# Kernel tuning notes

Measured on AMD Instinct MI355X. Metric: run time of the kernel, lower is better.

## Reference

```python
import jax, jax.numpy as jnp
import numpy as np

IMG = 800.0
STRIDES = (4, 8, 16, 32)
SIZES = (32.0, 64.0, 128.0, 256.0)
RATIOS = (0.5, 1.0, 2.0)
A = 3
PRE_NMS_K = 1000
POST_NMS = 512
NMS_TH = 0.7
POOL = 7
_MEAN = np.array([0.485, 0.456, 0.406], np.float32).reshape(3, 1, 1)
_STD = np.array([0.229, 0.224, 0.225], np.float32).reshape(3, 1, 1)


def _conv(x, w, stride=1):
    # x: [C,H,W], w: [O,I,kh,kw]
    return jax.lax.conv_general_dilated(x[None], w, (stride, stride), 'SAME',
                                        dimension_numbers=('NCHW', 'OIHW', 'NCHW'))[0]


def _make_anchors(fh, fw, stride, size):
    cy = (np.arange(fh, dtype=np.float32) + 0.5) * stride
    cx = (np.arange(fw, dtype=np.float32) + 0.5) * stride
    ws = np.array([size / np.sqrt(r) for r in RATIOS], np.float32)
    hs = np.array([size * np.sqrt(r) for r in RATIOS], np.float32)
    gy, gx = np.meshgrid(cy, cx, indexing='ij')
    x1 = gx[..., None] - ws / 2; y1 = gy[..., None] - hs / 2
    x2 = gx[..., None] + ws / 2; y2 = gy[..., None] + hs / 2
    return jnp.asarray(np.stack([x1, y1, x2, y2], -1).reshape(-1, 4))  # [fh*fw*A,4]


def _decode(anchors, deltas):
    aw = anchors[:, 2] - anchors[:, 0]; ah = anchors[:, 3] - anchors[:, 1]
    acx = anchors[:, 0] + aw * 0.5; acy = anchors[:, 1] + ah * 0.5
    dw = jnp.clip(deltas[:, 2], -4.0, 4.0); dh = jnp.clip(deltas[:, 3], -4.0, 4.0)
    cx = acx + deltas[:, 0] * aw; cy = acy + deltas[:, 1] * ah
    w = aw * jnp.exp(dw); h = ah * jnp.exp(dh)
    boxes = jnp.stack([cx - w * 0.5, cy - h * 0.5, cx + w * 0.5, cy + h * 0.5], -1)
    return jnp.clip(boxes, 0.0, IMG)


def _nms(boxes, scores, iou_th, max_out):
    # Greedy NMS with fixed output size (jit-compatible).
    x1, y1, x2, y2 = boxes[:, 0], boxes[:, 1], boxes[:, 2], boxes[:, 3]
    areas = (x2 - x1) * (y2 - y1)

    def body(i, state):
        s, keep = state
        idx = jnp.argmax(s)
        keep = keep.at[i].set(idx)
        ix1 = jnp.maximum(x1, x1[idx]); iy1 = jnp.maximum(y1, y1[idx])
        ix2 = jnp.minimum(x2, x2[idx]); iy2 = jnp.minimum(y2, y2[idx])
        inter = jnp.maximum(ix2 - ix1, 0.0) * jnp.maximum(iy2 - iy1, 0.0)
        iou = inter / (areas + areas[idx] - inter + 1e-6)
        return jnp.where(iou > iou_th, -jnp.inf, s), keep

    _, keep = jax.lax.fori_loop(0, max_out, body, (scores, jnp.zeros(max_out, jnp.int32)))
    return keep


def _roi_align(feat, rois, scale):
    # feat: [C,H,W]; rois: [N,4] in image coords; bilinear, 1 sample per bin.
    C, H, W = feat.shape
    n = rois.shape[0]
    x1 = rois[:, 0] * scale; y1 = rois[:, 1] * scale
    bw = (rois[:, 2] - rois[:, 0]) * scale / POOL
    bh = (rois[:, 3] - rois[:, 1]) * scale / POOL
    j = jnp.arange(POOL, dtype=feat.dtype) + 0.5
    gx = jnp.broadcast_to((x1[:, None] + j * bw[:, None] - 0.5)[:, None, :], (n, POOL, POOL))
    gy = jnp.broadcast_to((y1[:, None] + j * bh[:, None] - 0.5)[:, :, None], (n, POOL, POOL))
    fx = jnp.clip(jnp.floor(gx), 0.0, W - 1); fy = jnp.clip(jnp.floor(gy), 0.0, H - 1)
    x0 = fx.astype(jnp.int32); y0 = fy.astype(jnp.int32)
    x1i = jnp.minimum(x0 + 1, W - 1); y1i = jnp.minimum(y0 + 1, H - 1)
    wx = jnp.clip(gx - fx, 0.0, 1.0); wy = jnp.clip(gy - fy, 0.0, 1.0)
    v = (feat[:, y0, x0] * (1 - wy) * (1 - wx) + feat[:, y0, x1i] * (1 - wy) * wx
         + feat[:, y1i, x0] * wy * (1 - wx) + feat[:, y1i, x1i] * wy * wx)  # [C,N,P,P]
    return jnp.transpose(v, (1, 0, 2, 3))  # [N,C,P,P]


def _forward(x, stem_w, c2_w, c3_w, c4_w, c5_w, fpn2_w, fpn3_w, fpn4_w, fpn5_w,
             rpn_w, rpn_cls_w, rpn_box_w, fc1_w, fc1_b, fc2_w, fc2_b,
             cls_w, cls_b, breg_w, breg_b):
    x = (x - _MEAN) / _STD  # ImageNet normalize
    h = jax.nn.relu(_conv(x, stem_w, 2))      # [64,400,400]
    c2 = jax.nn.relu(_conv(h, c2_w, 2))       # [256,200,200] stride 4
    c3 = jax.nn.relu(_conv(c2, c3_w, 2))      # stride 8
    c4 = jax.nn.relu(_conv(c3, c4_w, 2))      # stride 16
    c5 = jax.nn.relu(_conv(c4, c5_w, 2))      # stride 32
    feats = [_conv(c2, fpn2_w), _conv(c3, fpn3_w), _conv(c4, fpn4_w), _conv(c5, fpn5_w)]

    boxes_l, scores_l = [], []
    for lvl, f in enumerate(feats):
        t = jax.nn.relu(_conv(f, rpn_w))
        fh, fw = f.shape[1], f.shape[2]
        logits = jnp.transpose(_conv(t, rpn_cls_w), (1, 2, 0)).reshape(-1)  # [fh*fw*A]
        deltas = jnp.transpose(_conv(t, rpn_box_w).reshape(A, 4, fh, fw), (2, 3, 0, 1)).reshape(-1, 4)
        anchors = _make_anchors(fh, fw, STRIDES[lvl], SIZES[lvl])
        dec = _decode(anchors, deltas)
        k = min(PRE_NMS_K, logits.shape[0])
        sc, idx = jax.lax.top_k(logits, k)
        boxes_l.append(dec[idx]); scores_l.append(sc)

    boxes = jnp.concatenate(boxes_l, 0)
    scores = jnp.concatenate(scores_l, 0)
    keep = _nms(boxes, scores, NMS_TH, POST_NMS)
    props = boxes[keep]  # [POST_NMS,4]

    pooled = _roi_align(feats[0], props, 1.0 / STRIDES[0])  # [N,256,7,7]
    v = pooled.reshape(POST_NMS, -1)
    v = jax.nn.relu(v @ fc1_w + fc1_b)
    v = jax.nn.relu(v @ fc2_w + fc2_b)
    return v @ cls_w + cls_b, v @ breg_w + breg_b, props, scores[keep]


def setup_inputs() -> dict:
    key = jax.random.key(0)
    ks = jax.random.split(key, 18)

    def he(k, shape):
        fan_in = int(np.prod(shape[1:])) if len(shape) == 4 else shape[0]
        return jax.random.normal(k, shape, jnp.float32) * float(np.sqrt(2.0 / fan_in))

    inp = {'x': jax.random.uniform(ks[0], (3, 800, 800), jnp.float32)}
    inp['stem_w'] = he(ks[1], (64, 3, 7, 7))
    inp['c2_w'] = he(ks[2], (256, 64, 3, 3))
    for i, name in enumerate(['c3_w', 'c4_w', 'c5_w', 'fpn2_w', 'fpn3_w', 'fpn4_w', 'fpn5_w', 'rpn_w']):
        inp[name] = he(ks[3 + i], (256, 256, 3, 3))
    inp['rpn_cls_w'] = he(ks[11], (3, 256, 1, 1))
    inp['rpn_box_w'] = he(ks[12], (12, 256, 1, 1))
    inp['fc1_w'] = he(ks[13], (12544, 1024)); inp['fc1_b'] = jnp.zeros((1024,), jnp.float32)
    inp['fc2_w'] = he(ks[14], (1024, 1024)); inp['fc2_b'] = jnp.zeros((1024,), jnp.float32)
    inp['cls_w'] = he(ks[15], (1024, 2)); inp['cls_b'] = jnp.zeros((2,), jnp.float32)
    inp['breg_w'] = he(ks[16], (1024, 8)); inp['breg_b'] = jnp.zeros((8,), jnp.float32)
    return inp


def reference(x, stem_w, c2_w, c3_w, c4_w, c5_w, fpn2_w, fpn3_w, fpn4_w, fpn5_w,
              rpn_w, rpn_cls_w, rpn_box_w, fc1_w, fc1_b, fc2_w, fc2_b,
              cls_w, cls_b, breg_w, breg_b):
    return _forward(x, stem_w, c2_w, c3_w, c4_w, c5_w, fpn2_w, fpn3_w, fpn4_w, fpn5_w,
                    rpn_w, rpn_cls_w, rpn_box_w, fc1_w, fc1_b, fc2_w, fc2_b,
                    cls_w, cls_b, breg_w, breg_b)
```

## Files before the change

### kernel.cpp

```cpp
#include <hip/hip_runtime.h>
#include <math.h>


#define DI __device__ __forceinline__

typedef short short8 __attribute__((ext_vector_type(8)));
typedef float float16v __attribute__((ext_vector_type(16)));

DI unsigned fkey(float f) {
  unsigned u = __float_as_uint(f);
  return (u & 0x80000000u) ? ~u : (u | 0x80000000u);
}

DI unsigned short f2bf(float f) {
  unsigned u = __float_as_uint(f);
  unsigned r = (u + 0x7FFFu + ((u >> 16) & 1u)) >> 16;
  return (unsigned short)r;
}

__global__ __launch_bounds__(256) void stem_conv(const float* __restrict__ x,
                                                 const float* __restrict__ w,
                                                 float* __restrict__ out) {
  __shared__ float tin[3 * 37 * 37];
  __shared__ float tw[4 * 147];
  const int x0 = blockIdx.x * 16, y0 = blockIdx.y * 16, co0 = blockIdx.z * 4;
  const int tid = threadIdx.x;
  for (int i = tid; i < 4 * 147; i += 256) tw[i] = w[co0 * 147 + i];
  const int ix0 = x0 * 2 - 2, iy0 = y0 * 2 - 2;
  const float mean[3] = {0.485f, 0.456f, 0.406f};
  const float stdv[3] = {0.229f, 0.224f, 0.225f};
  for (int i = tid; i < 3 * 37 * 37; i += 256) {
    int c = i / 1369, r = i % 1369, yy = r / 37, xx = r % 37;
    int gy = iy0 + yy, gx = ix0 + xx;
    float v = 0.f;
    if ((unsigned)gy < 800u && (unsigned)gx < 800u)
      v = __fdiv_rn(__fsub_rn(x[c * 640000 + gy * 800 + gx], mean[c]), stdv[c]);
    tin[i] = v;
  }
  __syncthreads();
  const int tx = tid & 15, ty = tid >> 4;
  float acc[4] = {0.f, 0.f, 0.f, 0.f};
  for (int c = 0; c < 3; ++c)
    for (int ky = 0; ky < 7; ++ky)
#pragma unroll
      for (int kx = 0; kx < 7; ++kx) {
        float v = tin[c * 1369 + (ty * 2 + ky) * 37 + (tx * 2 + kx)];
#pragma unroll
        for (int co = 0; co < 4; ++co)
          acc[co] = fmaf(v, tw[co * 147 + c * 49 + ky * 7 + kx], acc[co]);
      }
  int ox = x0 + tx, oy = y0 + ty;
#pragma unroll
  for (int co = 0; co < 4; ++co)
    out[(size_t)(co0 + co) * 160000 + oy * 400 + ox] = fmaxf(acc[co], 0.f);
}

__global__ void repack_w32(const float* __restrict__ w,
                           float* __restrict__ wpk, int Cin) {
  int i = blockIdx.x * 256 + threadIdx.x;
  int total = 16 * Cin * 9 * 16;
  if (i >= total) return;
  int co = i & 15;
  int r = i >> 4;
  int kk = r % 9;
  int r2 = r / 9;
  int ci = r2 % Cin;
  int z = r2 / Cin;
  wpk[i] = w[((size_t)(z * 16 + co) * Cin + ci) * 9 + kk];
}

template <int CHUNK, bool RELU>
__global__ __launch_bounds__(256) void conv32_db(
    const float* __restrict__ in, const float* __restrict__ wpk,
    float* __restrict__ out, int Cin, int Hin, int Win, int Hout, int Wout) {
  constexpr int TILE = CHUNK * 612;
  constexpr int NS = (TILE + 255) / 256;
  constexpr int PADT = NS * 256;
  __shared__ __align__(16) float tin2[2][PADT];
  const int tid = threadIdx.x;
  const int tx = tid & 15, ty = tid >> 4;
  const int x0 = blockIdx.x * 32, y0 = blockIdx.y * 16;
  const int ix0 = x0 - 1, iy0 = y0 - 1;
  const size_t HWin = (size_t)Hin * Win;

  int goff[NS];
#pragma unroll
  for (int j = 0; j < NS; ++j) {
    int e = j * 256 + tid;
    int c = e / 612, r = e % 612;
    int yy = r / 34, xx = r % 34;
    int gy = iy0 + yy, gx = ix0 + xx;
    bool ok = (e < TILE) && ((unsigned)gy < (unsigned)Hin) &&
              ((unsigned)gx < (unsigned)Win);
    goff[j] = ok ? (int)((size_t)c * HWin + (size_t)gy * Win + gx) : -1;
  }

  float acc0[16], acc1[16];
#pragma unroll
  for (int co = 0; co < 16; ++co) { acc0[co] = 0.f; acc1[co] = 0.f; }

  float stg[NS];
#pragma unroll
  for (int j = 0; j < NS; ++j)
    stg[j] = (goff[j] >= 0) ? in[goff[j]] : 0.f;
#pragma unroll
  for (int j = 0; j < NS; ++j) tin2[0][j * 256 + tid] = stg[j];
  __syncthreads();

  int buf = 0;
  for (int cb = 0; cb < Cin; cb += CHUNK) {
    const bool more = (cb + CHUNK) < Cin;
    if (more) {
      const float* gsrc = in + (size_t)(cb + CHUNK) * HWin;
#pragma unroll
      for (int j = 0; j < NS; ++j)
        stg[j] = (goff[j] >= 0) ? gsrc[goff[j]] : 0.f;
    }
    for (int ci = 0; ci < CHUNK; ++ci) {
      const float4* wq = (const float4*)(wpk +
          ((size_t)blockIdx.z * Cin + (size_t)(cb + ci)) * 144);
#pragma unroll
      for (int ky = 0; ky < 3; ++ky) {
        const float* tb = &tin2[buf][ci * 612 + (ty + ky) * 34 + 2 * tx];
        float2 d0 = *(const float2*)tb;
        float2 d1 = *(const float2*)(tb + 2);
#pragma unroll
        for (int kx = 0; kx < 3; ++kx) {
          float v0 = (kx == 0) ? d0.x : (kx == 1) ? d0.y : d1.x;
          float v1 = (kx == 0) ? d0.y : (kx == 1) ? d1.x : d1.y;
          const int kk = ky * 3 + kx;
          float4 w0 = wq[kk * 4 + 0];
          float4 w1 = wq[kk * 4 + 1];
          float4 w2 = wq[kk * 4 + 2];
          float4 w3 = wq[kk * 4 + 3];
          acc0[0]  = fmaf(v0, w0.x, acc0[0]);
          acc0[1]  = fmaf(v0, w0.y, acc0[1]);
          acc0[2]  = fmaf(v0, w0.z, acc0[2]);
          acc0[3]  = fmaf(v0, w0.w, acc0[3]);
          acc1[0]  = fmaf(v1, w0.x, acc1[0]);
          acc1[1]  = fmaf(v1, w0.y, acc1[1]);
          acc1[2]  = fmaf(v1, w0.z, acc1[2]);
          acc1[3]  = fmaf(v1, w0.w, acc1[3]);
          acc0[4]  = fmaf(v0, w1.x, acc0[4]);
          acc0[5]  = fmaf(v0, w1.y, acc0[5]);
          acc0[6]  = fmaf(v0, w1.z, acc0[6]);
          acc0[7]  = fmaf(v0, w1.w, acc0[7]);
          acc1[4]  = fmaf(v1, w1.x, acc1[4]);
          acc1[5]  = fmaf(v1, w1.y, acc1[5]);
          acc1[6]  = fmaf(v1, w1.z, acc1[6]);
          acc1[7]  = fmaf(v1, w1.w, acc1[7]);
          acc0[8]  = fmaf(v0, w2.x, acc0[8]);
          acc0[9]  = fmaf(v0, w2.y, acc0[9]);
          acc0[10] = fmaf(v0, w2.z, acc0[10]);
          acc0[11] = fmaf(v0, w2.w, acc0[11]);
          acc1[8]  = fmaf(v1, w2.x, acc1[8]);
          acc1[9]  = fmaf(v1, w2.y, acc1[9]);
          acc1[10] = fmaf(v1, w2.z, acc1[10]);
          acc1[11] = fmaf(v1, w2.w, acc1[11]);
          acc0[12] = fmaf(v0, w3.x, acc0[12]);
          acc0[13] = fmaf(v0, w3.y, acc0[13]);
          acc0[14] = fmaf(v0, w3.z, acc0[14]);
          acc0[15] = fmaf(v0, w3.w, acc0[15]);
          acc1[12] = fmaf(v1, w3.x, acc1[12]);
          acc1[13] = fmaf(v1, w3.y, acc1[13]);
          acc1[14] = fmaf(v1, w3.z, acc1[14]);
          acc1[15] = fmaf(v1, w3.w, acc1[15]);
        }
      }
    }
    if (more) {
#pragma unroll
      for (int j = 0; j < NS; ++j) tin2[buf ^ 1][j * 256 + tid] = stg[j];
    }
    __syncthreads();
    buf ^= 1;
  }

  const int co0 = blockIdx.z * 16;
  int oy = y0 + ty;
  if (oy < Hout) {
    int ox = x0 + 2 * tx;
    if (ox + 1 < Wout) {
#pragma unroll
      for (int co = 0; co < 16; ++co) {
        float a = acc0[co], b = acc1[co];
        if (RELU) { a = fmaxf(a, 0.f); b = fmaxf(b, 0.f); }
        float2 st; st.x = a; st.y = b;
        *(float2*)&out[(size_t)(co0 + co) * Hout * Wout +
                       (size_t)oy * Wout + ox] = st;
      }
    } else if (ox < Wout) {
#pragma unroll
      for (int co = 0; co < 16; ++co) {
        float a = acc0[co];
        if (RELU) a = fmaxf(a, 0.f);
        out[(size_t)(co0 + co) * Hout * Wout + (size_t)oy * Wout + ox] = a;
      }
    }
  }
}

template <int CHUNK, bool RELU>
__global__ __launch_bounds__(256) void conv16_s1(const float* __restrict__ in,
                                                 const float* __restrict__ wpk,
                                                 float* __restrict__ out,
                                                 int Cin, int Hin, int Win,
                                                 int Hout, int Wout) {
  constexpr int P = 24;
  constexpr int TOT = CHUNK * 18 * 18;
  constexpr int NS = (TOT + 255) / 256;
  __shared__ __align__(16) float tin[CHUNK * 18 * P];
  const int tid = threadIdx.x;
  const int tx = tid & 15, ty = tid >> 4;
  const int x0 = blockIdx.x * 16, y0 = blockIdx.y * 16;
  const int ix0 = x0 - 1, iy0 = y0 - 1;
  const size_t HWin = (size_t)Hin * Win;

  int goff[NS], loff[NS];
#pragma unroll
  for (int j = 0; j < NS; ++j) {
    int i = tid + j * 256;
    int c = i / 324, r = i % 324;
    int yy = r / 18, xx = r % 18;
    int gy = iy0 + yy, gx = ix0 + xx;
    bool ok = (i < TOT) && ((unsigned)gy < (unsigned)Hin) &&
              ((unsigned)gx < (unsigned)Win);
    goff[j] = ok ? (int)(c * HWin + (size_t)gy * Win + gx) : -1;
    loff[j] = c * 18 * P + yy * P + xx;
  }

  float acc[16];
#pragma unroll
  for (int co = 0; co < 16; ++co) acc[co] = 0.f;

  for (int cb = 0; cb < Cin; cb += CHUNK) {
    const size_t gbase = (size_t)cb * HWin;
#pragma unroll
    for (int j = 0; j < NS; ++j) {
      int i = tid + j * 256;
      if (i < TOT) {
        float v = 0.f;
        if (goff[j] >= 0) v = in[gbase + goff[j]];
        tin[loff[j]] = v;
      }
    }
    __syncthreads();
    for (int ci = 0; ci < CHUNK; ++ci) {
      const float4* wq = (const float4*)(wpk +
          ((size_t)blockIdx.z * Cin + (size_t)(cb + ci)) * 144);
#pragma unroll
      for (int ky = 0; ky < 3; ++ky) {
#pragma unroll
        for (int kx = 0; kx < 3; ++kx) {
          const int kk = ky * 3 + kx;
          float v = tin[ci * 18 * P + (ty + ky) * P + tx + kx];
          float4 w0 = wq[kk * 4 + 0];
          float4 w1 = wq[kk * 4 + 1];
          float4 w2 = wq[kk * 4 + 2];
          float4 w3 = wq[kk * 4 + 3];
          acc[0]  = fmaf(v, w0.x, acc[0]);
          acc[1]  = fmaf(v, w0.y, acc[1]);
          acc[2]  = fmaf(v, w0.z, acc[2]);
          acc[3]  = fmaf(v, w0.w, acc[3]);
          acc[4]  = fmaf(v, w1.x, acc[4]);
          acc[5]  = fmaf(v, w1.y, acc[5]);
          acc[6]  = fmaf(v, w1.z, acc[6]);
          acc[7]  = fmaf(v, w1.w, acc[7]);
          acc[8]  = fmaf(v, w2.x, acc[8]);
          acc[9]  = fmaf(v, w2.y, acc[9]);
          acc[10] = fmaf(v, w2.z, acc[10]);
          acc[11] = fmaf(v, w2.w, acc[11]);
          acc[12] = fmaf(v, w3.x, acc[12]);
          acc[13] = fmaf(v, w3.y, acc[13]);
          acc[14] = fmaf(v, w3.z, acc[14]);
          acc[15] = fmaf(v, w3.w, acc[15]);
        }
      }
    }
    __syncthreads();
  }
  const int co0 = blockIdx.z * 16;
  int oy = y0 + ty, ox = x0 + tx;
  if (oy < Hout && ox < Wout) {
#pragma unroll
    for (int co = 0; co < 16; ++co) {
      float v = acc[co];
      if (RELU) v = fmaxf(v, 0.f);
      out[(size_t)(co0 + co) * Hout * Wout + (size_t)oy * Wout + ox] = v;
    }
  }
}

template <int CHUNK, bool RELU>
__global__ __launch_bounds__(256) void conv16_s2(const float* __restrict__ in,
                                                 const float* __restrict__ wpk,
                                                 float* __restrict__ out,
                                                 int Cin, int Hin, int Win,
                                                 int Hout, int Wout) {
  constexpr int P = 20;
  constexpr int HALF = CHUNK * 33 * P;
  constexpr int TOT = CHUNK * 33 * 33;
  constexpr int NS = (TOT + 255) / 256;
  __shared__ __align__(16) float tin2[2 * HALF];
  const int tid = threadIdx.x;
  const int tx = tid & 15, ty = tid >> 4;
  const int x0 = blockIdx.x * 16, y0 = blockIdx.y * 16;
  const int ix0 = x0 * 2, iy0 = y0 * 2;
  const size_t HWin = (size_t)Hin * Win;

  int goff[NS], loff[NS];
#pragma unroll
  for (int j = 0; j < NS; ++j) {
    int i = tid + j * 256;
    int c = i / 1089, r = i % 1089;
    int yy = r / 33, xx = r % 33;
    int gy = iy0 + yy, gx = ix0 + xx;
    bool ok = (i < TOT) && ((unsigned)gy < (unsigned)Hin) &&
              ((unsigned)gx < (unsigned)Win);
    goff[j] = ok ? (int)(c * HWin + (size_t)gy * Win + gx) : -1;
    loff[j] = c * 33 * P + yy * P + (xx >> 1) + ((xx & 1) ? HALF : 0);
  }

  float acc[16];
#pragma unroll
  for (int co = 0; co < 16; ++co) acc[co] = 0.f;

  for (int cb = 0; cb < Cin; cb += CHUNK) {
    const size_t gbase = (size_t)cb * HWin;
#pragma unroll
    for (int j = 0; j < NS; ++j) {
      int i = tid + j * 256;
      if (i < TOT) {
        float v = 0.f;
        if (goff[j] >= 0) v = in[gbase + goff[j]];
        tin2[loff[j]] = v;
      }
    }
    __syncthreads();
    for (int ci = 0; ci < CHUNK; ++ci) {
      const float4* wq = (const float4*)(wpk +
          ((size_t)blockIdx.z * Cin + (size_t)(cb + ci)) * 144);
#pragma unroll
      for (int ky = 0; ky < 3; ++ky) {
#pragma unroll
        for (int kx = 0; kx < 3; ++kx) {
          const int kk = ky * 3 + kx;
          const float* base = (kx == 1) ? (tin2 + HALF) : tin2;
          const int cadd = (kx == 2) ? 1 : 0;
          float v = base[ci * 33 * P + (2 * ty + ky) * P + tx + cadd];
          float4 w0 = wq[kk * 4 + 0];
          float4 w1 = wq[kk * 4 + 1];
          float4 w2 = wq[kk * 4 + 2];
          float4 w3 = wq[kk * 4 + 3];
          acc[0]  = fmaf(v, w0.x, acc[0]);
          acc[1]  = fmaf(v, w0.y, acc[1]);
          acc[2]  = fmaf(v, w0.z, acc[2]);
          acc[3]  = fmaf(v, w0.w, acc[3]);
          acc[4]  = fmaf(v, w1.x, acc[4]);
          acc[5]  = fmaf(v, w1.y, acc[5]);
          acc[6]  = fmaf(v, w1.z, acc[6]);
          acc[7]  = fmaf(v, w1.w, acc[7]);
          acc[8]  = fmaf(v, w2.x, acc[8]);
          acc[9]  = fmaf(v, w2.y, acc[9]);
          acc[10] = fmaf(v, w2.z, acc[10]);
          acc[11] = fmaf(v, w2.w, acc[11]);
          acc[12] = fmaf(v, w3.x, acc[12]);
          acc[13] = fmaf(v, w3.y, acc[13]);
          acc[14] = fmaf(v, w3.z, acc[14]);
          acc[15] = fmaf(v, w3.w, acc[15]);
        }
      }
    }
    __syncthreads();
  }
  const int co0 = blockIdx.z * 16;
  int oy = y0 + ty, ox = x0 + tx;
  if (oy < Hout && ox < Wout) {
#pragma unroll
    for (int co = 0; co < 16; ++co) {
      float v = acc[co];
      if (RELU) v = fmaxf(v, 0.f);
      out[(size_t)(co0 + co) * Hout * Wout + (size_t)oy * Wout + ox] = v;
    }
  }
}

__global__ __launch_bounds__(256) void transpose_t(const float* __restrict__ in,
                                                   float* __restrict__ out,
                                                   int npix) {
  __shared__ float tile[32][33];
  const int p0 = blockIdx.x * 32, c0 = blockIdx.y * 32;
  const int tx = threadIdx.x & 31, ty = threadIdx.x >> 5;
  for (int r = ty; r < 32; r += 8) {
    int p = p0 + tx;
    tile[r][tx] = (p < npix) ? in[(size_t)(c0 + r) * npix + p] : 0.f;
  }
  __syncthreads();
  for (int r = ty; r < 32; r += 8) {
    int p = p0 + r;
    if (p < npix) out[(size_t)p * 256 + c0 + tx] = tile[tx][r];
  }
}

__global__ __launch_bounds__(256) void rpn_head_decode(
    const float* __restrict__ tt, const float* __restrict__ wcls,
    const float* __restrict__ wbox, float* __restrict__ boxes,
    float* __restrict__ scores, int fh, int fw, float stride, float ws0,
    float ws1, float ws2, float hs0, float hs1, float hs2) {
  __shared__ __align__(16) float wcs[256][16];
  for (int i = threadIdx.x; i < 256 * 16; i += 256) {
    int c = i & 255, o = i >> 8;
    float v = 0.f;
    if (o < 3) v = wcls[o * 256 + c];
    else if (o < 15) v = wbox[(o - 3) * 256 + c];
    wcs[c][o] = v;
  }
  __syncthreads();
  const int npix = fh * fw;
  int p = blockIdx.x * 256 + threadIdx.x;
  if (p >= npix) return;
  float a[15];
#pragma unroll
  for (int o = 0; o < 15; ++o) a[o] = 0.f;
  const float4* tp = (const float4*)(tt + (size_t)p * 256);
#pragma unroll 4
  for (int c4 = 0; c4 < 64; ++c4) {
    float4 tv = tp[c4];
#pragma unroll
    for (int j = 0; j < 4; ++j) {
      float v = (j == 0) ? tv.x : (j == 1) ? tv.y : (j == 2) ? tv.z : tv.w;
      int c = c4 * 4 + j;
      const float4* wr = (const float4*)&wcs[c][0];
      float4 w0 = wr[0], w1 = wr[1], w2 = wr[2], w3 = wr[3];
      a[0] = fmaf(v, w0.x, a[0]);   a[1] = fmaf(v, w0.y, a[1]);
      a[2] = fmaf(v, w0.z, a[2]);   a[3] = fmaf(v, w0.w, a[3]);
      a[4] = fmaf(v, w1.x, a[4]);   a[5] = fmaf(v, w1.y, a[5]);
      a[6] = fmaf(v, w1.z, a[6]);   a[7] = fmaf(v, w1.w, a[7]);
      a[8] = fmaf(v, w2.x, a[8]);   a[9] = fmaf(v, w2.y, a[9]);
      a[10] = fmaf(v, w2.z, a[10]); a[11] = fmaf(v, w2.w, a[11]);
      a[12] = fmaf(v, w3.x, a[12]); a[13] = fmaf(v, w3.y, a[13]);
      a[14] = fmaf(v, w3.z, a[14]);
    }
  }
  const int i = p / fw, j = p % fw;
  const float acy0 = __fmul_rn((float)i + 0.5f, stride);
  const float acx0 = __fmul_rn((float)j + 0.5f, stride);
  const float WS[3] = {ws0, ws1, ws2}, HS[3] = {hs0, hs1, hs2};
#pragma unroll
  for (int an = 0; an < 3; ++an) {
    float hw = __fmul_rn(WS[an], 0.5f), hh = __fmul_rn(HS[an], 0.5f);
    float x1a = __fsub_rn(acx0, hw), x2a = __fadd_rn(acx0, hw);
    float y1a = __fsub_rn(acy0, hh), y2a = __fadd_rn(acy0, hh);
    float aw = __fsub_rn(x2a, x1a), ah = __fsub_rn(y2a, y1a);
    float acx = __fadd_rn(x1a, __fmul_rn(aw, 0.5f));
    float acy = __fadd_rn(y1a, __fmul_rn(ah, 0.5f));
    float dx = a[3 + an * 4 + 0], dy = a[3 + an * 4 + 1];
    float dw = fminf(fmaxf(a[3 + an * 4 + 2], -4.f), 4.f);
    float dh = fminf(fmaxf(a[3 + an * 4 + 3], -4.f), 4.f);
    float cx = __fadd_rn(acx, __fmul_rn(dx, aw));
    float cy = __fadd_rn(acy, __fmul_rn(dy, ah));
    float w_ = __fmul_rn(aw, expf(dw));
    float h_ = __fmul_rn(ah, expf(dh));
    int idx = p * 3 + an;
    boxes[idx * 4 + 0] =
        fminf(fmaxf(__fsub_rn(cx, __fmul_rn(w_, 0.5f)), 0.f), 800.f);
    boxes[idx * 4 + 1] =
        fminf(fmaxf(__fsub_rn(cy, __fmul_rn(h_, 0.5f)), 0.f), 800.f);
    boxes[idx * 4 + 2] =
        fminf(fmaxf(__fadd_rn(cx, __fmul_rn(w_, 0.5f)), 0.f), 800.f);
    boxes[idx * 4 + 3] =
        fminf(fmaxf(__fadd_rn(cy, __fmul_rn(h_, 0.5f)), 0.f), 800.f);
    scores[idx] = a[an];
  }
}

__global__ void hist_hi_kernel(const float* __restrict__ s, int n,
                               int* __restrict__ hist) {
  int i = blockIdx.x * blockDim.x + threadIdx.x;
  if (i < n) atomicAdd(&hist[fkey(s[i]) >> 16], 1);
}

__global__ void hist_lo_kernel(const float* __restrict__ s, int n,
                               const int* __restrict__ sel,
                               int* __restrict__ hist) {
  unsigned b = (unsigned)sel[0];
  int i = blockIdx.x * blockDim.x + threadIdx.x;
  if (i < n) {
    unsigned key = fkey(s[i]);
    if ((key >> 16) == b) atomicAdd(&hist[key & 0xffffu], 1);
  }
}

__global__ __launch_bounds__(256) void scan_hi_kernel(
    const int* __restrict__ hist, int k, int* __restrict__ sel) {
  __shared__ int csum[256];
  int t = threadIdx.x;
  int s = 0;
  for (int i = 0; i < 256; ++i) s += hist[t * 256 + i];
  csum[t] = s;
  __syncthreads();
  if (t == 0) {
    int cum = 0;
    for (int c = 255; c >= 0; --c) {
      if (cum + csum[c] >= k) {
        int cc = cum;
        for (int b = c * 256 + 255;; --b) {
          int h = hist[b];
          if (cc + h >= k) {
            sel[0] = b; sel[1] = k - cc; sel[2] = cc;
            return;
          }
          cc += h;
        }
      }
      cum += csum[c];
    }
    sel[0] = 0; sel[1] = k - cum; sel[2] = cum;
  }
}

__global__ __launch_bounds__(256) void scan_lo_kernel(
    const int* __restrict__ hist, int* __restrict__ sel) {
  __shared__ int csum[256];
  int t = threadIdx.x;
  int s = 0;
  for (int i = 0; i < 256; ++i) s += hist[t * 256 + i];
  csum[t] = s;
  __syncthreads();
  if (t == 0) {
    int r = sel[1], b = sel[0], cc_hi = sel[2];
    int cum = 0;
    for (int c = 255; c >= 0; --c) {
      if (cum + csum[c] >= r) {
        int cc = cum;
        for (int l = c * 256 + 255;; --l) {
          int h = hist[l];
          if (cc + h >= r) {
            sel[3] = (int)(((unsigned)b << 16) | (unsigned)l);
            sel[4] = cc_hi + cc;
            sel[5] = r - cc;
            sel[6] = 0;
            sel[7] = 0;
            return;
          }
          cc += h;
        }
      }
      cum += csum[c];
    }
    sel[3] = (int)((unsigned)b << 16);
    sel[4] = cc_hi; sel[5] = r; sel[6] = 0; sel[7] = 0;
  }
}

__global__ void compact_kernel(const float* __restrict__ s,
                               const float* __restrict__ boxes, int n,
                               int* __restrict__ sel, float* __restrict__ out_s,
                               float* __restrict__ out_b, int obase) {
  int i = blockIdx.x * blockDim.x + threadIdx.x;
  if (i >= n) return;
  unsigned key = fkey(s[i]);
  unsigned kth = (unsigned)sel[3];
  int pos = -1;
  if (key > kth) {
    pos = atomicAdd(&sel[6], 1);
  } else if (key == kth) {
    int e = atomicAdd(&sel[7], 1);
    if (e < sel[5]) pos = sel[4] + e;
  }
  if (pos >= 0) {
    int o = obase + pos;
    out_s[o] = s[i];
    out_b[o * 4 + 0] = boxes[i * 4 + 0];
    out_b[o * 4 + 1] = boxes[i * 4 + 1];
    out_b[o * 4 + 2] = boxes[i * 4 + 2];
    out_b[o * 4 + 3] = boxes[i * 4 + 3];
  }
}

#define NMS_N 4000
#define NMS_W 63

__global__ __launch_bounds__(256) void rank_kernel(const float* __restrict__ s,
                                                   int* __restrict__ order) {
  __shared__ float ls[NMS_N];
  for (int i = threadIdx.x; i < NMS_N; i += 256) ls[i] = s[i];
  __syncthreads();
  int i = blockIdx.x * 256 + threadIdx.x;
  if (i >= NMS_N) return;
  float si = ls[i];
  int cnt = 0;
  for (int j = 0; j < NMS_N; ++j) {
    float sj = ls[j];
    cnt += (sj > si) || (sj == si && j < i);
  }
  order[cnt] = i;
}

__global__ __launch_bounds__(256) void supp_kernel(
    const float* __restrict__ boxes, unsigned long long* __restrict__ supp) {
  __shared__ float sx1[NMS_W * 64], sy1[NMS_W * 64];
  __shared__ float sx2[NMS_W * 64], sy2[NMS_W * 64];
  for (int i = threadIdx.x; i < NMS_W * 64; i += 256) {
    float x1 = 0.f, y1 = 0.f, x2 = 0.f, y2 = 0.f;
    if (i < NMS_N) {
      x1 = boxes[i * 4 + 0]; y1 = boxes[i * 4 + 1];
      x2 = boxes[i * 4 + 2]; y2 = boxes[i * 4 + 3];
    }
    sx1[i] = x1; sy1[i] = y1; sx2[i] = x2; sy2[i] = y2;
  }
  __syncthreads();
  const int wave = threadIdx.x >> 6, lane = threadIdx.x & 63;
  for (int rr = 0; rr < 16; ++rr) {
    int i = blockIdx.x * 16 + rr;
    if (i >= NMS_N) return;
    float ix1 = sx1[i], iy1 = sy1[i], ix2 = sx2[i], iy2 = sy2[i];
    float ia = __fmul_rn(__fsub_rn(ix2, ix1), __fsub_rn(iy2, iy1));
    for (int w = wave; w < NMS_W; w += 4) {
      int j = w * 64 + lane;
      float jx1 = sx1[j], jy1 = sy1[j], jx2 = sx2[j], jy2 = sy2[j];
      float ja = __fmul_rn(__fsub_rn(jx2, jx1), __fsub_rn(jy2, jy1));
      float cx1 = fmaxf(jx1, ix1), cy1 = fmaxf(jy1, iy1);
      float cx2 = fminf(jx2, ix2), cy2 = fminf(jy2, iy2);
      float iw = fmaxf(__fsub_rn(cx2, cx1), 0.f);
      float ih = fmaxf(__fsub_rn(cy2, cy1), 0.f);
      float inter = __fmul_rn(iw, ih);
      float denom = __fadd_rn(__fsub_rn(__fadd_rn(ja, ia), inter), 1e-6f);
      bool pred = __fdiv_rn(inter, denom) > 0.7f;
      unsigned long long bits = __ballot(pred);
      if (lane == 0) supp[(size_t)i * NMS_W + w] = bits;
    }
  }
}

__global__ __launch_bounds__(64) void nms_scan(
    const unsigned long long* __restrict__ supp, const int* __restrict__ order,
    const float* __restrict__ boxes, const float* __restrict__ scores,
    float* __restrict__ props, float* __restrict__ out_props,
    float* __restrict__ out_scores) {
  __shared__ unsigned long long removed[NMS_W];
  __shared__ int keepL[512];
  const int tid = threadIdx.x;
  if (tid < NMS_W) removed[tid] = 0ull;
  __syncthreads();
  int kept = 0, sticky = -1;
  for (int g = 0; g < NMS_W && sticky < 0 && kept < 512; ++g) {
    int pos = g * 64 + tid;
    int c = (pos < NMS_N) ? order[pos] : -1;
    while (kept < 512) {
      bool avail = (c >= 0) && !((removed[c >> 6] >> (c & 63)) & 1ull);
      unsigned long long bal = __ballot(avail);
      if (bal == 0ull) break;
      int fl = __ffsll((unsigned long long)bal) - 1;
      int ck = __shfl(c, fl);
      if (tid == 0) keepL[kept] = ck;
      kept++;
      unsigned long long w =
          (tid < NMS_W) ? supp[(size_t)ck * NMS_W + tid] : 0ull;
      unsigned long long selfw = __shfl(w, ck >> 6);
      if (tid < NMS_W) removed[tid] |= w;
      __syncthreads();
      if (!((selfw >> (ck & 63)) & 1ull)) { sticky = ck; break; }
    }
  }
  __syncthreads();
  const int fill = (sticky >= 0) ? sticky : 0;
  for (int k = tid; k < 512; k += 64) {
    int idx = (k < kept) ? keepL[k] : fill;
    float x1 = boxes[idx * 4 + 0], y1 = boxes[idx * 4 + 1];
    float x2 = boxes[idx * 4 + 2], y2 = boxes[idx * 4 + 3];
    props[k * 4 + 0] = x1; props[k * 4 + 1] = y1;
    props[k * 4 + 2] = x2; props[k * 4 + 3] = y2;
    out_props[k * 4 + 0] = x1; out_props[k * 4 + 1] = y1;
    out_props[k * 4 + 2] = x2; out_props[k * 4 + 3] = y2;
    out_scores[k] = scores[idx];
  }
}

__global__ __launch_bounds__(256) void roi_align_kernel(
    const float* __restrict__ feat, const float* __restrict__ rois,
    float* __restrict__ out) {
  __shared__ int sx0[7], sx1i[7], sy0[7], sy1i[7];
  __shared__ float swx[7], swy[7];
  const int n = blockIdx.x;
  if (threadIdx.x < 14) {
    int i = threadIdx.x % 7;
    bool isY = threadIdx.x >= 7;
    float r0 = rois[n * 4 + (isY ? 1 : 0)];
    float r1 = rois[n * 4 + (isY ? 3 : 2)];
    float a = __fmul_rn(r0, 0.25f);
    float b = __fdiv_rn(__fmul_rn(__fsub_rn(r1, r0), 0.25f), 7.0f);
    float g = __fsub_rn(__fadd_rn(a, __fmul_rn((float)i + 0.5f, b)), 0.5f);
    float fl = fminf(fmaxf(floorf(g), 0.f), 199.f);
    int i0 = (int)fl;
    int i1 = min(i0 + 1, 199);
    float wf = fminf(fmaxf(__fsub_rn(g, fl), 0.f), 1.f);
    if (isY) { sy0[i] = i0; sy1i[i] = i1; swy[i] = wf; }
    else     { sx0[i] = i0; sx1i[i] = i1; swx[i] = wf; }
  }
  __syncthreads();
  const int c = threadIdx.x;
  const float* fc_ = feat + (size_t)c * 40000;
  float* o = out + (size_t)n * 12544 + c * 49;
  for (int s = 0; s < 49; ++s) {
    int py = s / 7, px = s % 7;
    int y0 = sy0[py], y1 = sy1i[py], x0 = sx0[px], x1 = sx1i[px];
    float wy = swy[py], wx = swx[px];
    float v00 = fc_[y0 * 200 + x0], v01 = fc_[y0 * 200 + x1];
    float v10 = fc_[y1 * 200 + x0], v11 = fc_[y1 * 200 + x1];
    float v = ((v00 * (1.f - wy)) * (1.f - wx)) + ((v01 * (1.f - wy)) * wx) +
              ((v10 * wy) * (1.f - wx)) + ((v11 * wy) * wx);
    o[s] = v;
  }
}

__global__ void cast_a(const float* __restrict__ in,
                       unsigned short* __restrict__ out, int n) {
  int i = blockIdx.x * 256 + threadIdx.x;
  if (i < n) out[i] = f2bf(in[i]);
}

__global__ __launch_bounds__(256) void cast_bt(const float* __restrict__ B,
                                               unsigned short* __restrict__ Bt,
                                               int K, int N) {
  __shared__ float tile[32][33];
  const int k0 = blockIdx.y * 32, n0 = blockIdx.x * 32;
  const int tx = threadIdx.x & 31, ty = threadIdx.x >> 5;
  for (int r = ty; r < 32; r += 8)
    tile[r][tx] = B[(size_t)(k0 + r) * N + n0 + tx];
  __syncthreads();
  for (int r = ty; r < 32; r += 8)
    Bt[(size_t)(n0 + r) * K + k0 + tx] = f2bf(tile[tx][r]);
}

__global__ __launch_bounds__(256) void fc_mfma(
    const unsigned short* __restrict__ A,
    const unsigned short* __restrict__ Bt,
    float* __restrict__ Cp, int M, int N, int K, int kLen) {
  const int tid = threadIdx.x;
  const int lane = tid & 63, wave = tid >> 6;
  const int n = lane & 31, half = lane >> 5;
  const int bm = blockIdx.y * 128 + wave * 32;
  const int bn = blockIdx.x * 64;
  const int k0s = blockIdx.z * kLen;
  const unsigned short* arow = A + (size_t)(bm + n) * K + half * 8;
  const unsigned short* b0row = Bt + (size_t)(bn + n) * K + half * 8;
  const unsigned short* b1row = Bt + (size_t)(bn + 32 + n) * K + half * 8;
  float16v acc0, acc1;
#pragma unroll
  for (int r = 0; r < 16; ++r) { acc0[r] = 0.f; acc1[r] = 0.f; }
  for (int k0 = k0s; k0 < k0s + kLen; k0 += 16) {
    short8 a = *(const short8*)(arow + k0);
    short8 b0 = *(const short8*)(b0row + k0);
    short8 b1 = *(const short8*)(b1row + k0);
    acc0 = __builtin_amdgcn_mfma_f32_32x32x16_bf16(a, b0, acc0, 0, 0, 0);
    acc1 = __builtin_amdgcn_mfma_f32_32x32x16_bf16(a, b1, acc1, 0, 0, 0);
  }
  float* Cz = Cp + (size_t)blockIdx.z * M * N;
#pragma unroll
  for (int r = 0; r < 16; ++r) {
    int row = bm + (r & 3) + 8 * (r >> 2) + 4 * half;
    Cz[(size_t)row * N + bn + n] = acc0[r];
    Cz[(size_t)row * N + bn + 32 + n] = acc1[r];
  }
}

__global__ void fc_combine(const float* __restrict__ p,
                           const float* __restrict__ bias,
                           float* __restrict__ out, int MN, int N, int S) {
  int i = blockIdx.x * 256 + threadIdx.x;
  if (i >= MN) return;
  float v = 0.f;
  for (int s = 0; s < S; ++s) v += p[(size_t)s * MN + i];
  out[i] = fmaxf(v + bias[i % N], 0.f);
}

__global__ __launch_bounds__(64) void heads_kernel(
    const float* __restrict__ v, const float* __restrict__ wc,
    const float* __restrict__ bc, const float* __restrict__ wb,
    const float* __restrict__ bbias, float* __restrict__ out) {
  const int m = blockIdx.x;
  const int lane = threadIdx.x;
  float acc[10];
#pragma unroll
  for (int o = 0; o < 10; ++o) acc[o] = 0.f;
  for (int k = lane; k < 1024; k += 64) {
    float x = v[(size_t)m * 1024 + k];
    acc[0] = fmaf(x, wc[k * 2 + 0], acc[0]);
    acc[1] = fmaf(x, wc[k * 2 + 1], acc[1]);
#pragma unroll
    for (int o = 0; o < 8; ++o) acc[2 + o] = fmaf(x, wb[k * 8 + o], acc[2 + o]);
  }
#pragma unroll
  for (int off = 32; off > 0; off >>= 1)
#pragma unroll
    for (int o = 0; o < 10; ++o) acc[o] += __shfl_down(acc[o], off);
  if (lane == 0) {
    out[m * 2 + 0] = acc[0] + bc[0];
    out[m * 2 + 1] = acc[1] + bc[1];
#pragma unroll
    for (int o = 0; o < 8; ++o) out[1024 + m * 8 + o] = acc[2 + o] + bbias[o];
  }
}

extern "C" void kernel_launch(void* const* d_in, const int* in_sizes, int n_in,
                              void* d_out, int out_size, void* d_ws,
                              size_t ws_size, hipStream_t stream) {
  const float* x      = (const float*)d_in[0];
  const float* w_stem = (const float*)d_in[1];
  const float* w_c2   = (const float*)d_in[2];
  const float* w_c3   = (const float*)d_in[3];
  const float* w_c4   = (const float*)d_in[4];
  const float* w_c5   = (const float*)d_in[5];
  const float* w_f2   = (const float*)d_in[6];
  const float* w_f3   = (const float*)d_in[7];
  const float* w_f4   = (const float*)d_in[8];
  const float* w_f5   = (const float*)d_in[9];
  const float* w_rpn  = (const float*)d_in[10];
  const float* w_cls  = (const float*)d_in[11];
  const float* w_box  = (const float*)d_in[12];
  const float* w_fc1  = (const float*)d_in[13];
  const float* b_fc1  = (const float*)d_in[14];
  const float* w_fc2  = (const float*)d_in[15];
  const float* b_fc2  = (const float*)d_in[16];
  const float* w_clsh = (const float*)d_in[17];
  const float* b_clsh = (const float*)d_in[18];
  const float* w_breg = (const float*)d_in[19];
  const float* b_breg = (const float*)d_in[20];
  float* dout = (float*)d_out;

  float* ws = (float*)d_ws;
  float* stem = ws;
  float* c2   = stem + 10240000;
  float* c3   = c2 + 10240000;
  float* c4   = c3 + 2560000;
  float* c5   = c4 + 640000;
  float* f2   = c5 + 160000;
  float* f3   = f2 + 10240000;
  float* f4   = f3 + 2560000;
  float* f5   = f4 + 640000;
  float* boxes_all  = f5 + 160000;
  float* scores_all = boxes_all + 16000;
  float* props      = scores_all + 4000;
  int*   hist = (int*)(props + 2048);
  int*   sel  = hist + 65536;
  float* wpkA = (float*)(sel + 16);
  float* wpkB = wpkA + 589824;
  float* wpkC = wpkB + 589824;
  float* wpkD = wpkC + 589824;
  float* wpkE = wpkD + 147456;
  float* wpkF = wpkE + 589824;
  float* wpkG = wpkF + 589824;
  float* wpkH = wpkG + 589824;
  float* wpkI = wpkH + 589824;
  float* t      = c2;
  float* tt     = stem;
  float* dec    = c3;
  float* slvl   = c4;
  int*   order  = (int*)c3;
  unsigned long long* supp =
      (unsigned long long*)(c3 + 8192);
  float* pooled = stem;
  float* fc1o   = stem + 6422528;
  float* fc2o   = fc1o + 524288;
  float* fcp    = fc2o + 524288;
  unsigned short* Abf1 = (unsigned short*)c2;
  unsigned short* Bt1  = (unsigned short*)(c2 + 3211264);
  unsigned short* Abf2 = (unsigned short*)c3;
  unsigned short* Bt2  = (unsigned short*)(c3 + 262144);

  repack_w32<<<2304, 256, 0, stream>>>(w_f2, wpkA, 256);
  repack_w32<<<2304, 256, 0, stream>>>(w_f3, wpkB, 256);
  repack_w32<<<2304, 256, 0, stream>>>(w_rpn, wpkC, 256);
  repack_w32<<<576, 256, 0, stream>>>(w_c2, wpkD, 64);
  repack_w32<<<2304, 256, 0, stream>>>(w_c3, wpkE, 256);
  repack_w32<<<2304, 256, 0, stream>>>(w_c4, wpkF, 256);
  repack_w32<<<2304, 256, 0, stream>>>(w_c5, wpkG, 256);
  repack_w32<<<2304, 256, 0, stream>>>(w_f4, wpkH, 256);
  repack_w32<<<2304, 256, 0, stream>>>(w_f5, wpkI, 256);

  stem_conv<<<dim3(25, 25, 16), 256, 0, stream>>>(x, w_stem, stem);
  conv16_s2<4, true><<<dim3(13, 13, 16), 256, 0, stream>>>(
      stem, wpkD, c2, 64, 400, 400, 200, 200);
  conv16_s2<4, true><<<dim3(7, 7, 16), 256, 0, stream>>>(
      c2, wpkE, c3, 256, 200, 200, 100, 100);
  conv16_s2<4, true><<<dim3(4, 4, 16), 256, 0, stream>>>(
      c3, wpkF, c4, 256, 100, 100, 50, 50);
  conv16_s2<4, true><<<dim3(2, 2, 16), 256, 0, stream>>>(
      c4, wpkG, c5, 256, 50, 50, 25, 25);
  conv32_db<4, false><<<dim3(7, 13, 16), 256, 0, stream>>>(
      c2, wpkA, f2, 256, 200, 200, 200, 200);
  conv32_db<4, false><<<dim3(4, 7, 16), 256, 0, stream>>>(
      c3, wpkB, f3, 256, 100, 100, 100, 100);
  conv16_s1<8, false><<<dim3(4, 4, 16), 256, 0, stream>>>(
      c4, wpkH, f4, 256, 50, 50, 50, 50);
  conv16_s1<8, false><<<dim3(2, 2, 16), 256, 0, stream>>>(
      c5, wpkI, f5, 256, 25, 25, 25, 25);

  const float* feats[4] = {f2, f3, f4, f5};
  const int dims[4] = {200, 100, 50, 25};
  const float strds[4] = {4.f, 8.f, 16.f, 32.f};
  const double szs[4] = {32.0, 64.0, 128.0, 256.0};
  for (int lvl = 0; lvl < 4; ++lvl) {
    const int d = dims[lvl];
    const int npix = d * d;
    const int N = npix * 3;
    if (lvl == 0)
      conv32_db<4, true><<<dim3(7, 13, 16), 256, 0, stream>>>(
          feats[lvl], wpkC, t, 256, d, d, d, d);
    else if (lvl == 1)
      conv32_db<4, true><<<dim3(4, 7, 16), 256, 0, stream>>>(
          feats[lvl], wpkC, t, 256, d, d, d, d);
    else if (lvl == 2)
      conv16_s1<8, true><<<dim3(4, 4, 16), 256, 0, stream>>>(
          feats[lvl], wpkC, t, 256, d, d, d, d);
    else
      conv16_s1<8, true><<<dim3(2, 2, 16), 256, 0, stream>>>(
          feats[lvl], wpkC, t, 256, d, d, d, d);
    transpose_t<<<dim3((npix + 31) / 32, 8), 256, 0, stream>>>(t, tt, npix);
    double sz = szs[lvl];
    float ws0 = (float)(sz / sqrt(0.5)), ws1 = (float)sz,
          ws2 = (float)(sz / sqrt(2.0));
    float hs0 = (float)(sz * sqrt(0.5)), hs1 = (float)sz,
          hs2 = (float)(sz * sqrt(2.0));
    rpn_head_decode<<<(npix + 255) / 256, 256, 0, stream>>>(
        tt, w_cls, w_box, dec, slvl, d, d, strds[lvl], ws0, ws1, ws2, hs0, hs1,
        hs2);
    hipMemsetAsync(hist, 0, 65536 * sizeof(int), stream);
    hist_hi_kernel<<<(N + 255) / 256, 256, 0, stream>>>(slvl, N, hist);
    scan_hi_kernel<<<1, 256, 0, stream>>>(hist, 1000, sel);
    hipMemsetAsync(hist, 0, 65536 * sizeof(int), stream);
    hist_lo_kernel<<<(N + 255) / 256, 256, 0, stream>>>(slvl, N, sel, hist);
    scan_lo_kernel<<<1, 256, 0, stream>>>(hist, sel);
    compact_kernel<<<(N + 255) / 256, 256, 0, stream>>>(
        slvl, dec, N, sel, scores_all, boxes_all, lvl * 1000);
  }

  rank_kernel<<<16, 256, 0, stream>>>(scores_all, order);
  supp_kernel<<<250, 256, 0, stream>>>(boxes_all, supp);
  nms_scan<<<1, 64, 0, stream>>>(supp, order, boxes_all, scores_all, props,
                                 dout + 5120, dout + 7168);

  roi_align_kernel<<<512, 256, 0, stream>>>(f2, props, pooled);
  cast_a<<<(6422528 + 255) / 256, 256, 0, stream>>>(pooled, Abf1, 6422528);
  cast_bt<<<dim3(32, 392), 256, 0, stream>>>(w_fc1, Bt1, 12544, 1024);
  fc_mfma<<<dim3(16, 4, 4), 256, 0, stream>>>(Abf1, Bt1, fcp, 512, 1024, 12544,
                                              3136);
  fc_combine<<<2048, 256, 0, stream>>>(fcp, b_fc1, fc1o, 524288, 1024, 4);
  cast_a<<<(524288 + 255) / 256, 256, 0, stream>>>(fc1o, Abf2, 524288);
  cast_bt<<<dim3(32, 32), 256, 0, stream>>>(w_fc2, Bt2, 1024, 1024);
  fc_mfma<<<dim3(16, 4, 4), 256, 0, stream>>>(Abf2, Bt2, fcp, 512, 1024, 1024,
                                              256);
  fc_combine<<<2048, 256, 0, stream>>>(fcp, b_fc2, fc2o, 524288, 1024, 4);
  heads_kernel<<<512, 64, 0, stream>>>(fc2o, w_clsh, b_clsh, w_breg, b_breg,
                                       dout);
}
```

Before: 5.303 ms.

## Merge weight repacks into one launch and batch lateral convs per launch

```diff
diff --git a/kernel.cpp b/kernel.cpp
--- a/kernel.cpp
+++ b/kernel.cpp
@@ -18,14 +18,61 @@
   return (unsigned short)r;
 }
 
+DI void rp256(const float* src, float* dst, int j) {
+  int co = j & 15; int r = j >> 4; int kk = r % 9; int r2 = r / 9;
+  int ci = r2 & 255; int z = r2 >> 8;
+  dst[j] = src[((size_t)(z * 16 + co) * 256 + ci) * 9 + kk];
+}
+
+__global__ void repack_all(
+    const float* __restrict__ wf2, const float* __restrict__ wf3,
+    const float* __restrict__ wrpn, const float* __restrict__ wc2,
+    const float* __restrict__ wc3, const float* __restrict__ wc4,
+    const float* __restrict__ wc5, const float* __restrict__ wf4,
+    const float* __restrict__ wf5, const float* __restrict__ wstem,
+    float* __restrict__ wpkA, float* __restrict__ wpkB,
+    float* __restrict__ wpkC, float* __restrict__ wpkD,
+    float* __restrict__ wpkE, float* __restrict__ wpkF,
+    float* __restrict__ wpkG, float* __restrict__ wpkH,
+    float* __restrict__ wpkI, float* __restrict__ wpkS) {
+  const int SZ = 589824, SZD = 147456;
+  const int D0 = 3 * SZ;
+  const int D1 = D0 + SZD;
+  const int D2 = D1 + 5 * SZ;
+  const int D3 = D2 + 9408;
+  int i = blockIdx.x * 256 + threadIdx.x;
+  if (i >= D3) return;
+  if (i < D0) {
+    const float* src = (i < SZ) ? wf2 : (i < 2 * SZ) ? wf3 : wrpn;
+    float* dst = (i < SZ) ? wpkA : (i < 2 * SZ) ? wpkB : wpkC;
+    rp256(src, dst, i % SZ);
+  } else if (i < D1) {
+    int j = i - D0;
+    int co = j & 15; int r = j >> 4; int kk = r % 9; int r2 = r / 9;
+    int ci = r2 & 63; int z = r2 >> 6;
+    wpkD[j] = wc2[((size_t)(z * 16 + co) * 64 + ci) * 9 + kk];
+  } else if (i < D2) {
+    int j = i - D1;
+    int seg = j / SZ; j -= seg * SZ;
+    const float* src = (seg == 0) ? wc3 : (seg == 1) ? wc4
+                       : (seg == 2) ? wc5 : (seg == 3) ? wf4 : wf5;
+    float* dst = (seg == 0) ? wpkE : (seg == 1) ? wpkF
+                 : (seg == 2) ? wpkG : (seg == 3) ? wpkH : wpkI;
+    rp256(src, dst, j);
+  } else {
+    int j = i - D2;
+    int co = j & 3; int r = j >> 2;
+    int k = r % 147; int z = r / 147;
+    wpkS[j] = wstem[(size_t)(z * 4 + co) * 147 + k];
+  }
+}
+
 __global__ __launch_bounds__(256) void stem_conv(const float* __restrict__ x,
-                                                 const float* __restrict__ w,
+                                                 const float* __restrict__ wpkS,
                                                  float* __restrict__ out) {
   __shared__ float tin[3 * 37 * 37];
-  __shared__ float tw[4 * 147];
   const int x0 = blockIdx.x * 16, y0 = blockIdx.y * 16, co0 = blockIdx.z * 4;
   const int tid = threadIdx.x;
-  for (int i = tid; i < 4 * 147; i += 256) tw[i] = w[co0 * 147 + i];
   const int ix0 = x0 * 2 - 2, iy0 = y0 * 2 - 2;
   const float mean[3] = {0.485f, 0.456f, 0.406f};
   const float stdv[3] = {0.229f, 0.224f, 0.225f};
@@ -40,14 +87,17 @@
   __syncthreads();
   const int tx = tid & 15, ty = tid >> 4;
   float acc[4] = {0.f, 0.f, 0.f, 0.f};
+  const float4* wq = (const float4*)(wpkS + (size_t)blockIdx.z * 588);
   for (int c = 0; c < 3; ++c)
     for (int ky = 0; ky < 7; ++ky)
 #pragma unroll
       for (int kx = 0; kx < 7; ++kx) {
         float v = tin[c * 1369 + (ty * 2 + ky) * 37 + (tx * 2 + kx)];
-#pragma unroll
-        for (int co = 0; co < 4; ++co)
-          acc[co] = fmaf(v, tw[co * 147 + c * 49 + ky * 7 + kx], acc[co]);
+        float4 wv = wq[c * 49 + ky * 7 + kx];
+        acc[0] = fmaf(v, wv.x, acc[0]);
+        acc[1] = fmaf(v, wv.y, acc[1]);
+        acc[2] = fmaf(v, wv.z, acc[2]);
+        acc[3] = fmaf(v, wv.w, acc[3]);
       }
   int ox = x0 + tx, oy = y0 + ty;
 #pragma unroll
@@ -55,31 +105,16 @@
     out[(size_t)(co0 + co) * 160000 + oy * 400 + ox] = fmaxf(acc[co], 0.f);
 }
 
-__global__ void repack_w32(const float* __restrict__ w,
-                           float* __restrict__ wpk, int Cin) {
-  int i = blockIdx.x * 256 + threadIdx.x;
-  int total = 16 * Cin * 9 * 16;
-  if (i >= total) return;
-  int co = i & 15;
-  int r = i >> 4;
-  int kk = r % 9;
-  int r2 = r / 9;
-  int ci = r2 % Cin;
-  int z = r2 / Cin;
-  wpk[i] = w[((size_t)(z * 16 + co) * Cin + ci) * 9 + kk];
-}
-
 template <int CHUNK, bool RELU>
-__global__ __launch_bounds__(256) void conv32_db(
-    const float* __restrict__ in, const float* __restrict__ wpk,
-    float* __restrict__ out, int Cin, int Hin, int Win, int Hout, int Wout) {
+DI void conv32_body(const float* __restrict__ in,
+                    const float* __restrict__ wpk, float* __restrict__ out,
+                    int Cin, int Hin, int Win, int Hout, int Wout, int bx,
+                    int by, int bz, float (*tin2)[((CHUNK * 612 + 255) / 256) * 256]) {
   constexpr int TILE = CHUNK * 612;
   constexpr int NS = (TILE + 255) / 256;
-  constexpr int PADT = NS * 256;
-  __shared__ __align__(16) float tin2[2][PADT];
   const int tid = threadIdx.x;
   const int tx = tid & 15, ty = tid >> 4;
-  const int x0 = blockIdx.x * 32, y0 = blockIdx.y * 16;
+  const int x0 = bx * 32, y0 = by * 16;
   const int ix0 = x0 - 1, iy0 = y0 - 1;
   const size_t HWin = (size_t)Hin * Win;
 
@@ -118,7 +153,7 @@
     }
     for (int ci = 0; ci < CHUNK; ++ci) {
       const float4* wq = (const float4*)(wpk +
-          ((size_t)blockIdx.z * Cin + (size_t)(cb + ci)) * 144);
+          ((size_t)bz * Cin + (size_t)(cb + ci)) * 144);
 #pragma unroll
       for (int ky = 0; ky < 3; ++ky) {
         const float* tb = &tin2[buf][ci * 612 + (ty + ky) * 34 + 2 * tx];
@@ -176,7 +211,7 @@
     buf ^= 1;
   }
 
-  const int co0 = blockIdx.z * 16;
+  const int co0 = bz * 16;
   int oy = y0 + ty;
   if (oy < Hout) {
     int ox = x0 + 2 * tx;
@@ -201,18 +236,47 @@
 }
 
 template <int CHUNK, bool RELU>
-__global__ __launch_bounds__(256) void conv16_s1(const float* __restrict__ in,
-                                                 const float* __restrict__ wpk,
-                                                 float* __restrict__ out,
-                                                 int Cin, int Hin, int Win,
-                                                 int Hout, int Wout) {
+__global__ __launch_bounds__(256) void conv32_db(
+    const float* __restrict__ in, const float* __restrict__ wpk,
+    float* __restrict__ out, int Cin, int Hin, int Win, int Hout, int Wout) {
+  constexpr int PADT = ((CHUNK * 612 + 255) / 256) * 256;
+  __shared__ __align__(16) float tin2[2][PADT];
+  conv32_body<CHUNK, RELU>(in, wpk, out, Cin, Hin, Win, Hout, Wout,
+                           blockIdx.x, blockIdx.y, blockIdx.z, tin2);
+}
+
+template <int CHUNK>
+__global__ __launch_bounds__(256) void conv32_lat(
+    const float* __restrict__ inA, const float* __restrict__ wA,
+    float* __restrict__ oA, int CinA, int HA, int WA, int gxA, int gyA,
+    int nA, const float* __restrict__ inB, const float* __restrict__ wB,
+    float* __restrict__ oB, int CinB, int HB, int WB, int gxB, int gyB) {
+  constexpr int PADT = ((CHUNK * 612 + 255) / 256) * 256;
+  __shared__ __align__(16) float tin2[2][PADT];
+  int bid = blockIdx.x;
+  if (bid < nA) {
+    int bx = bid % gxA; int r = bid / gxA; int by = r % gyA; int bz = r / gyA;
+    conv32_body<CHUNK, false>(inA, wA, oA, CinA, HA, WA, HA, WA, bx, by, bz,
+                              tin2);
+  } else {
+    bid -= nA;
+    int bx = bid % gxB; int r = bid / gxB; int by = r % gyB; int bz = r / gyB;
+    conv32_body<CHUNK, false>(inB, wB, oB, CinB, HB, WB, HB, WB, bx, by, bz,
+                              tin2);
+  }
+}
+
+template <int CHUNK, bool RELU>
+DI void conv16s1_body(const float* __restrict__ in,
+                      const float* __restrict__ wpk, float* __restrict__ out,
+                      int Cin, int Hin, int Win, int Hout, int Wout, int bx,
+                      int by, int bz, float* tin) {
   constexpr int P = 24;
   constexpr int TOT = CHUNK * 18 * 18;
   constexpr int NS = (TOT + 255) / 256;
-  __shared__ __align__(16) float tin[CHUNK * 18 * P];
   const int tid = threadIdx.x;
   const int tx = tid & 15, ty = tid >> 4;
-  const int x0 = blockIdx.x * 16, y0 = blockIdx.y * 16;
+  const int x0 = bx * 16, y0 = by * 16;
   const int ix0 = x0 - 1, iy0 = y0 - 1;
   const size_t HWin = (size_t)Hin * Win;
 
@@ -247,7 +311,7 @@
     __syncthreads();
     for (int ci = 0; ci < CHUNK; ++ci) {
       const float4* wq = (const float4*)(wpk +
-          ((size_t)blockIdx.z * Cin + (size_t)(cb + ci)) * 144);
+          ((size_t)bz * Cin + (size_t)(cb + ci)) * 144);
 #pragma unroll
       for (int ky = 0; ky < 3; ++ky) {
 #pragma unroll
@@ -279,7 +343,7 @@
     }
     __syncthreads();
   }
-  const int co0 = blockIdx.z * 16;
+  const int co0 = bz * 16;
   int oy = y0 + ty, ox = x0 + tx;
   if (oy < Hout && ox < Wout) {
 #pragma unroll
@@ -288,6 +352,37 @@
       if (RELU) v = fmaxf(v, 0.f);
       out[(size_t)(co0 + co) * Hout * Wout + (size_t)oy * Wout + ox] = v;
     }
+  }
+}
+
+template <int CHUNK, bool RELU>
+__global__ __launch_bounds__(256) void conv16_s1(const float* __restrict__ in,
+                                                 const float* __restrict__ wpk,
+                                                 float* __restrict__ out,
+                                                 int Cin, int Hin, int Win,
+                                                 int Hout, int Wout) {
+  __shared__ __align__(16) float tin[CHUNK * 18 * 24];
+  conv16s1_body<CHUNK, RELU>(in, wpk, out, Cin, Hin, Win, Hout, Wout,
+                             blockIdx.x, blockIdx.y, blockIdx.z, tin);
+}
+
+template <int CHUNK>
+__global__ __launch_bounds__(256) void conv16_lat(
+    const float* __restrict__ inA, const float* __restrict__ wA,
+    float* __restrict__ oA, int CinA, int HA, int WA, int gxA, int gyA,
+    int nA, const float* __restrict__ inB, const float* __restrict__ wB,
+    float* __restrict__ oB, int CinB, int HB, int WB, int gxB, int gyB) {
+  __shared__ __align__(16) float tin[CHUNK * 18 * 24];
+  int bid = blockIdx.x;
+  if (bid < nA) {
+    int bx = bid % gxA; int r = bid / gxA; int by = r % gyA; int bz = r / gyA;
+    conv16s1_body<CHUNK, false>(inA, wA, oA, CinA, HA, WA, HA, WA, bx, by, bz,
+                                tin);
+  } else {
+    bid -= nA;
+    int bx = bid % gxB; int r = bid / gxB; int by = r % gyB; int bz = r / gyB;
+    conv16s1_body<CHUNK, false>(inB, wB, oB, CinB, HB, WB, HB, WB, bx, by, bz,
+                                tin);
   }
 }
 
@@ -853,6 +948,7 @@
   float* wpkG = wpkF + 589824;
   float* wpkH = wpkG + 589824;
   float* wpkI = wpkH + 589824;
+  float* wpkS = wpkI + 589824;
   float* t      = c2;
   float* tt     = stem;
   float* dec    = c3;
@@ -869,17 +965,11 @@
   unsigned short* Abf2 = (unsigned short*)c3;
   unsigned short* Bt2  = (unsigned short*)(c3 + 262144);
 
-  repack_w32<<<2304, 256, 0, stream>>>(w_f2, wpkA, 256);
-  repack_w32<<<2304, 256, 0, stream>>>(w_f3, wpkB, 256);
-  repack_w32<<<2304, 256, 0, stream>>>(w_rpn, wpkC, 256);
-  repack_w32<<<576, 256, 0, stream>>>(w_c2, wpkD, 64);
-  repack_w32<<<2304, 256, 0, stream>>>(w_c3, wpkE, 256);
-  repack_w32<<<2304, 256, 0, stream>>>(w_c4, wpkF, 256);
-  repack_w32<<<2304, 256, 0, stream>>>(w_c5, wpkG, 256);
-  repack_w32<<<2304, 256, 0, stream>>>(w_f4, wpkH, 256);
-  repack_w32<<<2304, 256, 0, stream>>>(w_f5, wpkI, 256);
-
-  stem_conv<<<dim3(25, 25, 16), 256, 0, stream>>>(x, w_stem, stem);
+  repack_all<<<19045, 256, 0, stream>>>(
+      w_f2, w_f3, w_rpn, w_c2, w_c3, w_c4, w_c5, w_f4, w_f5, w_stem,
+      wpkA, wpkB, wpkC, wpkD, wpkE, wpkF, wpkG, wpkH, wpkI, wpkS);
+
+  stem_conv<<<dim3(25, 25, 16), 256, 0, stream>>>(x, wpkS, stem);
   conv16_s2<4, true><<<dim3(13, 13, 16), 256, 0, stream>>>(
       stem, wpkD, c2, 64, 400, 400, 200, 200);
   conv16_s2<4, true><<<dim3(7, 7, 16), 256, 0, stream>>>(
@@ -888,14 +978,12 @@
       c3, wpkF, c4, 256, 100, 100, 50, 50);
   conv16_s2<4, true><<<dim3(2, 2, 16), 256, 0, stream>>>(
       c4, wpkG, c5, 256, 50, 50, 25, 25);
-  conv32_db<4, false><<<dim3(7, 13, 16), 256, 0, stream>>>(
-      c2, wpkA, f2, 256, 200, 200, 200, 200);
-  conv32_db<4, false><<<dim3(4, 7, 16), 256, 0, stream>>>(
-      c3, wpkB, f3, 256, 100, 100, 100, 100);
-  conv16_s1<8, false><<<dim3(4, 4, 16), 256, 0, stream>>>(
-      c4, wpkH, f4, 256, 50, 50, 50, 50);
-  conv16_s1<8, false><<<dim3(2, 2, 16), 256, 0, stream>>>(
-      c5, wpkI, f5, 256, 25, 25, 25, 25);
+  conv32_lat<4><<<1904, 256, 0, stream>>>(
+      c2, wpkA, f2, 256, 200, 200, 7, 13, 1456,
+      c3, wpkB, f3, 256, 100, 100, 4, 7);
+  conv16_lat<8><<<320, 256, 0, stream>>>(
+      c4, wpkH, f4, 256, 50, 50, 4, 4, 256,
+      c5, wpkI, f5, 256, 25, 25, 2, 2);
 
   const float* feats[4] = {f2, f3, f4, f5};
   const int dims[4] = {200, 100, 50, 25};
```

Measured after the change: 4.935 ms. 1.07x faster.
